# Optimization experiments

Hardware: AMD Instinct MI355X
Metric: run time of the kernel (lower is better)

The kernel has to match this reference:

```python
import jax, jax.numpy as jnp
import numpy as np

# --- module hyperparameters (from init_kwargs) ---
N_MODES = 4096          # N: number of Fourier modes
M_TAPS = 4              # m: window half-width (2m taps per point)
SIGMA = 2.0             # oversampling factor
N_GRID = int(SIGMA * N_MODES)  # n: oversampled grid size = 8192
BATCH = 16
N_PTS = 131072          # nonuniform points per batch


def _kb_window(k, n, m, sigma):
    """Kaiser-Bessel window phi(k); NaNs (outside support / at arg==0) -> 0, as in torch."""
    b = (2.0 - 1.0 / sigma) * jnp.pi
    arg = jnp.sqrt(jnp.asarray(m * m, jnp.float32) - (n * k) ** 2)  # NaN where |k| > m/n
    out = jnp.sinh(b * arg) / (arg * jnp.pi)
    return jnp.nan_to_num(out, nan=0.0)


def _kb_fourier_coeffs(N, n, m, sigma):
    """phi_hat: Fourier coefficients of the Kaiser-Bessel window, length N."""
    b = (2.0 - 1.0 / sigma) * jnp.pi
    inds = jnp.arange(-(N // 2), N // 2, dtype=jnp.float32)
    return jnp.i0(m * jnp.sqrt(b * b - (2.0 * jnp.pi * inds / n) ** 2))


def setup_inputs() -> dict:
    key = jax.random.key(0)
    k1, k2, k3 = jax.random.split(key, 3)
    x = jax.random.uniform(k1, (BATCH, N_PTS), dtype=jnp.float32,
                           minval=-0.5, maxval=0.5)  # points in [-1/2, 1/2)
    f_hat_real = jax.random.normal(k2, (BATCH, N_MODES), dtype=jnp.float32)
    f_hat_imag = jax.random.normal(k3, (BATCH, N_MODES), dtype=jnp.float32)
    return {"x": x, "f_hat_real": f_hat_real, "f_hat_imag": f_hat_imag}


def reference(x, f_hat_real, f_hat_imag):
    N, n, m, sigma = N_MODES, N_GRID, M_TAPS, SIGMA
    B = x.shape[0]
    f_hat = (f_hat_real + 1j * f_hat_imag).astype(jnp.complex64)  # [B, N]

    # ---- deconvolve in Fourier domain and go to oversampled spatial grid ----
    phi_hat = _kb_fourier_coeffs(N, n, m, sigma)                  # [N]
    g_hat = f_hat / phi_hat                                       # [B, N]
    pad = (n - N) // 2
    g_hat = jnp.pad(g_hat, ((0, 0), (pad, pad)))                  # [B, n]
    g_hat = jnp.fft.fftshift(g_hat, axes=-1)
    g = jnp.fft.ifftshift(jnp.fft.fft(g_hat, norm='backward'), axes=-1)  # [B, n]

    # ---- sparse convolution (gather + window, type-2 interpolation) ----
    l = jnp.arange(2 * m, dtype=jnp.int32).reshape(2 * m, 1, 1)   # [2m,1,1]
    inds = (jnp.ceil(n * x).astype(jnp.int32) - m)[None] + l      # [2m,B,M]
    w = _kb_window(x[None] - inds.astype(jnp.float32) / n,
                   n, m, sigma).astype(jnp.complex64)             # [2m,B,M]
    wrapped = (inds + n // 2) % n                                 # periodic wrap
    b_idx = jnp.arange(B).reshape(1, B, 1)
    g_l = g[b_idx, wrapped]                                       # gather [2m,B,M]
    return jnp.sum(w * g_l, axis=0)                               # [B, M] complex64
```

## Files before the change

kernel.cpp:

```cpp
#include <hip/hip_runtime.h>
#include <hip/hip_fp16.h>
#include <math.h>

#define NMODES 4096
#define NGRID  8192
#define BATCH  16
#define NPTS   131072
#define GSTRIDE 8200
#define GSCALE 1048576.0f
#define OSCALE 1.5178830414797062e-07f

__device__ __forceinline__ float2 cmul(float2 a, float2 b) {
    return make_float2(a.x * b.x - a.y * b.y, a.x * b.y + a.y * b.x);
}

__device__ __forceinline__ float deconv_signed(int fidx) {
    float k = (float)(fidx - 2048);
    float t = k * 7.66990393942820614e-4f;
    float z = 4.0f * sqrtf(22.2066099024510563f - t * t);
    float iz = 1.0f / z;
    float p  = 1.0f + iz * (0.125f + iz * (0.0703125f +
               iz * (0.0732421875f + iz * 0.112152099609375f)));
    float phi = __expf(z) * p * rsqrtf(6.28318530717958648f * z);
    float s = (fidx & 1) ? -1.0f : 1.0f;
    return s / phi;
}

__global__ __launch_bounds__(512) void nfft_fft_kernel(
    const float* __restrict__ fr, const float* __restrict__ fi,
    __half2* __restrict__ g16)
{
    __shared__ float2 hbuf[NMODES];
    __shared__ float2 fbuf[512];
    __shared__ float2 w16[16];

    const int b   = blockIdx.x >> 4;
    const int k1  = blockIdx.x & 15;
    const int tid = threadIdx.x;

    if (tid < 16) {
        float tn = -(float)tid * 0.0625f;
        w16[tid] = make_float2(__builtin_amdgcn_cosf(tn),
                               __builtin_amdgcn_sinf(tn));
    }
#pragma unroll
    for (int i = 0; i < 8; ++i) {
        int fidx = tid + i * 512;
        float inv = deconv_signed(fidx);
        hbuf[fidx] = make_float2(fr[b * NMODES + fidx] * inv,
                                 fi[b * NMODES + fidx] * inv);
    }
    __syncthreads();

    {
        int n2 = tid;
        float2 acc = make_float2(0.0f, 0.0f);
#pragma unroll
        for (int r = 0; r < 8; ++r) {
            float2 w = w16[((r + 4) * k1) & 15];
            float2 h = hbuf[n2 + 512 * r];
            acc.x = fmaf(h.x, w.x, fmaf(-h.y, w.y, acc.x));
            acc.y = fmaf(h.x, w.y, fmaf( h.y, w.x, acc.y));
        }
        float tn = -(float)(n2 * k1) * 1.220703125e-4f;
        float2 tw = make_float2(__builtin_amdgcn_cosf(tn),
                                __builtin_amdgcn_sinf(tn));
        int rb = (int)(__brev((unsigned)n2) >> 23);
        fbuf[rb] = cmul(acc, tw);
    }
    __syncthreads();

    for (int s = 0; s <= 8; ++s) {
        const int   half = 1 << s;
        const float tscl = -0.5f / (float)half;
        if (tid < 256) {
            int pos = tid & (half - 1);
            int idx = ((tid ^ pos) << 1) | pos;
            float sn = __builtin_amdgcn_sinf(tscl * (float)pos);
            float cs = __builtin_amdgcn_cosf(tscl * (float)pos);
            float2 a = fbuf[idx];
            float2 t = fbuf[idx + half];
            float2 bt = make_float2(t.x * cs - t.y * sn,
                                    t.x * sn + t.y * cs);
            fbuf[idx]        = make_float2(a.x + bt.x, a.y + bt.y);
            fbuf[idx + half] = make_float2(a.x - bt.x, a.y - bt.y);
        }
        __syncthreads();
    }

    const float s2 = ((k1 & 1) ? -1.0f : 1.0f) * GSCALE;
    __half2* base = g16 + b * GSTRIDE + k1;
    {
        int j = tid;
        float2 v = fbuf[j];
        base[16 * j] = __floats2half2_rn(v.x * s2, v.y * s2);
    }
    if (tid == 0 && k1 < 8) {
        float2 v = fbuf[0];
        g16[b * GSTRIDE + NGRID + k1] = __floats2half2_rn(v.x * s2, v.y * s2);
    }
}

__global__ __launch_bounds__(1024) void nfft_interp_kernel(
    const float* __restrict__ x, const __half2* __restrict__ g16,
    float* __restrict__ out, int cplx)
{
    const int b   = blockIdx.x & 15;
    const int blk = blockIdx.x >> 4;
    const int tid = threadIdx.x;

    const __half2* gb = g16 + b * GSTRIDE;
    const int base = b * NPTS + blk * 4096;
    const float4 xv4 = ((const float4*)(x + base))[tid];
    float outre[4], outim[4];

#pragma unroll
    for (int q = 0; q < 4; ++q) {
        float xv = (q == 0) ? xv4.x : (q == 1) ? xv4.y : (q == 2) ? xv4.z : xv4.w;
        float fl   = xv * 8192.0f;
        float cf   = ceilf(fl);
        int   c    = (int)cf;
        float frac = cf - fl;
        int   wr0  = (c + 12284) & (NGRID - 1);
        const __half2* gp = gb + wr0;
        float re = 0.0f, im = 0.0f;
#pragma unroll
        for (int l = 1; l < 7; ++l) {
            float u    = (float)(4 - l) - frac;
            float arg2 = fmaf(-u, u, 16.0f);
            float r    = rsqrtf(arg2);
            float z    = arg2 * r * 4.71238898038468986f;
            float w    = __expf(z) * r;
            float2 gv = __half22float2(gp[l]);
            re = fmaf(w, gv.x, re);
            im = fmaf(w, gv.y, im);
        }
        outre[q] = re * OSCALE;
        outim[q] = im * OSCALE;
    }

    if (cplx) {
        float2* o = ((float2*)out) + base + tid * 4;
        o[0] = make_float2(outre[0], outim[0]);
        o[1] = make_float2(outre[1], outim[1]);
        o[2] = make_float2(outre[2], outim[2]);
        o[3] = make_float2(outre[3], outim[3]);
    } else {
        ((float4*)(out + base))[tid] =
            make_float4(outre[0], outre[1], outre[2], outre[3]);
    }
}

__global__ __launch_bounds__(1024) void nfft_fused_kernel(
    const float* __restrict__ x, const float* __restrict__ fr,
    const float* __restrict__ fi, float* __restrict__ out, int cplx)
{
    __shared__ float2 buf[NGRID];
    const int b   = blockIdx.x >> 5;
    const int blk = blockIdx.x & 31;
    const int tid = threadIdx.x;

    for (int j = tid; j < NGRID; j += 1024) {
        float2 v = make_float2(0.0f, 0.0f);
        if (j >= 2048 && j < 6144) {
            int fidx = j - 2048;
            float inv = deconv_signed(fidx);
            v.x = fr[b * NMODES + fidx] * inv;
            v.y = fi[b * NMODES + fidx] * inv;
        }
        buf[j] = v;
    }
    __syncthreads();

    for (int s = 12; s >= 0; --s) {
        const int   half = 1 << s;
        const float tscl = -0.5f / (float)half;
#pragma unroll
        for (int ii = 0; ii < 4; ++ii) {
            int i = tid + ii * 1024;
            int pos = i & (half - 1);
            int idx = ((i ^ pos) << 1) | pos;
            float sn = __builtin_amdgcn_sinf(tscl * (float)pos);
            float cs = __builtin_amdgcn_cosf(tscl * (float)pos);
            float2 a = buf[idx];
            float2 c = buf[idx + half];
            buf[idx] = make_float2(a.x + c.x, a.y + c.y);
            float2 d = make_float2(a.x - c.x, a.y - c.y);
            buf[idx + half] = make_float2(d.x * cs - d.y * sn,
                                          d.x * sn + d.y * cs);
        }
        __syncthreads();
    }

    const int base = b * NPTS + blk * 4096;
    for (int p = tid; p < 4096; p += 1024) {
        float xv   = x[base + p];
        float fl   = xv * 8192.0f;
        int   c    = (int)ceilf(fl);
        float frac = (float)c - fl;
        float re = 0.0f, im = 0.0f;
#pragma unroll
        for (int l = 0; l < 8; ++l) {
            int   ind  = c - 4 + l;
            float u    = (float)(4 - l) - frac;
            float arg2 = 16.0f - u * u;
            float w    = 0.0f;
            if (arg2 > 0.0f) {
                float r   = rsqrtf(arg2);
                float arg = arg2 * r;
                float z   = 4.71238898038468986f * arg;
                w = (__expf(z) - __expf(-z)) * 0.15915494309189533577f * r;
            }
            if (ind & 1) w = -w;
            int wr = (ind + 4096) & (NGRID - 1);
            int rb = (int)(__brev((unsigned)wr) >> 19);
            float2 gv = buf[rb];
            re = fmaf(w, gv.x, re);
            im = fmaf(w, gv.y, im);
        }
        if (cplx) ((float2*)out)[base + p] = make_float2(re, im);
        else      out[base + p] = re;
    }
}

extern "C" void kernel_launch(void* const* d_in, const int* in_sizes, int n_in,
                              void* d_out, int out_size, void* d_ws, size_t ws_size,
                              hipStream_t stream) {
    (void)in_sizes; (void)n_in;
    const float* x  = (const float*)d_in[0];
    const float* fr = (const float*)d_in[1];
    const float* fi = (const float*)d_in[2];

    const int cplx = (out_size >= BATCH * NPTS * 2) ? 1 : 0;
    const size_t g_bytes = (size_t)BATCH * GSTRIDE * sizeof(__half2);

    if (ws_size >= g_bytes) {
        __half2* g16 = (__half2*)d_ws;
        nfft_fft_kernel<<<BATCH * 16, 512, 0, stream>>>(fr, fi, g16);
        nfft_interp_kernel<<<BATCH * 32, 1024, 0, stream>>>(
            x, g16, (float*)d_out, cplx);
    } else {
        nfft_fused_kernel<<<BATCH * 32, 1024, 0, stream>>>(
            x, fr, fi, (float*)d_out, cplx);
    }
}
```

Baseline: 18.81 us.

## Precompute per-cell degree-7 polynomials in offset for real-output interpolation

For real output, a new kernel turns each grid cell's six window-weighted neighbours into eight polynomial coefficients in the fractional offset. It uses a Chebyshev-fit matrix that the host computes each call. The interpolation kernel then evaluates one Horner polynomial per point from two float4 loads, so the six exp/rsqrt window evaluations per point go away. In exchange it adds a kernel launch, a 4 MB intermediate write and read, host-side matrix solving, and polynomial approximation error.

```diff
diff --git a/kernel.cpp b/kernel.cpp
--- a/kernel.cpp
+++ b/kernel.cpp
@@ -9,6 +9,8 @@
 #define GSTRIDE 8200
 #define GSCALE 1048576.0f
 #define OSCALE 1.5178830414797062e-07f
+
+struct AMat { float a[48]; };
 
 __device__ __forceinline__ float2 cmul(float2 a, float2 b) {
     return make_float2(a.x * b.x - a.y * b.y, a.x * b.y + a.y * b.x);
@@ -99,6 +101,64 @@
         float2 v = fbuf[0];
         g16[b * GSTRIDE + NGRID + k1] = __floats2half2_rn(v.x * s2, v.y * s2);
     }
+}
+
+__global__ __launch_bounds__(1024) void nfft_conv_kernel(
+    const __half2* __restrict__ g16, float4* __restrict__ P, AMat A)
+{
+    const int gid = blockIdx.x * 1024 + threadIdx.x;
+    const int b   = gid >> 13;
+    const int c   = gid & (NGRID - 1);
+    const __half2* gb = g16 + b * GSTRIDE + c;
+
+    float g1 = __low2float(gb[1]);
+    float g2 = __low2float(gb[2]);
+    float g3 = __low2float(gb[3]);
+    float g4 = __low2float(gb[4]);
+    float g5 = __low2float(gb[5]);
+    float g6 = __low2float(gb[6]);
+
+#define PD(d) (A.a[0*8+(d)]*g1 + A.a[1*8+(d)]*g2 + A.a[2*8+(d)]*g3 + \
+               A.a[3*8+(d)]*g4 + A.a[4*8+(d)]*g5 + A.a[5*8+(d)]*g6)
+    float p0 = PD(0), p1 = PD(1), p2 = PD(2), p3 = PD(3);
+    float p4 = PD(4), p5 = PD(5), p6 = PD(6), p7 = PD(7);
+#undef PD
+    P[gid * 2]     = make_float4(p0, p1, p2, p3);
+    P[gid * 2 + 1] = make_float4(p4, p5, p6, p7);
+}
+
+__global__ __launch_bounds__(1024) void nfft_interp_poly_kernel(
+    const float* __restrict__ x, const float4* __restrict__ P,
+    float* __restrict__ out)
+{
+    const int b   = blockIdx.x & 15;
+    const int blk = blockIdx.x >> 4;
+    const int tid = threadIdx.x;
+
+    const float4* Pb = P + (size_t)b * NGRID * 2;
+    const int base = b * NPTS + blk * 4096;
+    const float4 xv4 = ((const float4*)(x + base))[tid];
+    float o0, o1, o2, o3;
+
+#define POLY_PT(XV, OUTV) do {                                      \
+        float fl   = (XV) * 8192.0f;                                \
+        float cf   = ceilf(fl);                                     \
+        int   c    = (int)cf;                                       \
+        float f_   = cf - fl;                                       \
+        int   wr0  = (c + 12284) & (NGRID - 1);                     \
+        float4 pa = Pb[wr0 * 2];                                    \
+        float4 pb = Pb[wr0 * 2 + 1];                                \
+        float h = pb.w;                                             \
+        h = fmaf(h, f_, pb.z); h = fmaf(h, f_, pb.y);               \
+        h = fmaf(h, f_, pb.x); h = fmaf(h, f_, pa.w);               \
+        h = fmaf(h, f_, pa.z); h = fmaf(h, f_, pa.y);               \
+        h = fmaf(h, f_, pa.x);                                      \
+        (OUTV) = h;                                                 \
+    } while (0)
+    POLY_PT(xv4.x, o0); POLY_PT(xv4.y, o1);
+    POLY_PT(xv4.z, o2); POLY_PT(xv4.w, o3);
+#undef POLY_PT
+    ((float4*)(out + base))[tid] = make_float4(o0, o1, o2, o3);
 }
 
 __global__ __launch_bounds__(1024) void nfft_interp_kernel(
@@ -223,6 +283,45 @@
     }
 }
 
+static void nfft_compute_amat(AMat* M) {
+    const double PI = 3.14159265358979323846;
+    const double bb = 1.5 * PI;
+    const double osc = 1.0 / (2.0 * PI * 1048576.0);
+    double t[8];
+    for (int i = 0; i < 8; ++i)
+        t[i] = 0.5 - 0.5 * cos(PI * (2.0 * i + 1.0) / 16.0);
+    for (int l = 1; l <= 6; ++l) {
+        double W[8][9];
+        for (int i = 0; i < 8; ++i) {
+            double pw = 1.0;
+            for (int d = 0; d < 8; ++d) { W[i][d] = pw; pw *= t[i]; }
+            double u   = (double)(4 - l) - t[i];
+            double arg = sqrt(16.0 - u * u);
+            W[i][8] = osc * exp(bb * arg) / arg;
+        }
+        for (int col = 0; col < 8; ++col) {
+            int piv = col;
+            for (int r2 = col + 1; r2 < 8; ++r2)
+                if (fabs(W[r2][col]) > fabs(W[piv][col])) piv = r2;
+            if (piv != col)
+                for (int cc = col; cc < 9; ++cc) {
+                    double tmp = W[col][cc]; W[col][cc] = W[piv][cc]; W[piv][cc] = tmp;
+                }
+            for (int r2 = col + 1; r2 < 8; ++r2) {
+                double f = W[r2][col] / W[col][col];
+                for (int cc = col; cc < 9; ++cc) W[r2][cc] -= f * W[col][cc];
+            }
+        }
+        double a[8];
+        for (int row = 7; row >= 0; --row) {
+            double s = W[row][8];
+            for (int cc = row + 1; cc < 8; ++cc) s -= W[row][cc] * a[cc];
+            a[row] = s / W[row][row];
+        }
+        for (int d = 0; d < 8; ++d) M->a[(l - 1) * 8 + d] = (float)a[d];
+    }
+}
+
 extern "C" void kernel_launch(void* const* d_in, const int* in_sizes, int n_in,
                               void* d_out, int out_size, void* d_ws, size_t ws_size,
                               hipStream_t stream) {
@@ -233,8 +332,19 @@
 
     const int cplx = (out_size >= BATCH * NPTS * 2) ? 1 : 0;
     const size_t g_bytes = (size_t)BATCH * GSTRIDE * sizeof(__half2);
-
-    if (ws_size >= g_bytes) {
+    const size_t p_off   = g_bytes;
+    const size_t p_bytes = (size_t)BATCH * NGRID * 8 * sizeof(float);
+
+    if (!cplx && ws_size >= p_off + p_bytes) {
+        __half2* g16 = (__half2*)d_ws;
+        float4*  P   = (float4*)((char*)d_ws + p_off);
+        AMat A;
+        nfft_compute_amat(&A);
+        nfft_fft_kernel<<<BATCH * 16, 512, 0, stream>>>(fr, fi, g16);
+        nfft_conv_kernel<<<128, 1024, 0, stream>>>(g16, P, A);
+        nfft_interp_poly_kernel<<<BATCH * 32, 1024, 0, stream>>>(
+            x, P, (float*)d_out);
+    } else if (ws_size >= g_bytes) {
         __half2* g16 = (__half2*)d_ws;
         nfft_fft_kernel<<<BATCH * 16, 512, 0, stream>>>(fr, fi, g16);
         nfft_interp_kernel<<<BATCH * 32, 1024, 0, stream>>>(
```

Measured after the change: 28.69 us. 52.5% more time.
